# Kernel tuning notes

Hardware: AMD Instinct MI355X
Metric: run time of the kernel (lower is better)

The kernel has to match this reference:

```python
import jax, jax.numpy as jnp
import numpy as np

T, B, C, S = 1000, 64, 512, 100
BLANK = 0
SMOOTHING = 0.1
NEG = -1e30  # finite -inf sentinel (safe for logaddexp and grads)


def setup_inputs() -> dict:
    key = jax.random.key(0)
    k1, k2, k3 = jax.random.split(key, 3)
    logits = jax.random.normal(k1, (T, B, C), dtype=jnp.float32)
    # nn.CTCLoss expects log-probabilities over the class dim
    log_probs = jax.nn.log_softmax(logits, axis=-1)
    targets = jax.random.randint(k2, (B, S), 1, C, dtype=jnp.int32)  # avoid blank=0
    input_lengths = jnp.full((B,), T, dtype=jnp.int32)
    target_lengths = jax.random.randint(k3, (B,), S // 2, S + 1, dtype=jnp.int32)
    return {"log_probs": log_probs, "targets": targets,
            "input_lengths": input_lengths, "target_lengths": target_lengths}


def ctc_nll(log_probs, targets, input_lengths, target_lengths):
    """Per-sample CTC negative log-likelihood via log-domain alpha recursion."""
    Tt, Bb, Cc = log_probs.shape
    Ss = targets.shape[1]
    L = 2 * Ss + 1  # extended label sequence: blank t1 blank t2 ... blank
    ext = jnp.full((Bb, L), BLANK, dtype=targets.dtype).at[:, 1::2].set(targets)
    bidx = jnp.arange(Bb)[:, None]
    lp_ext = log_probs[:, bidx, ext]  # (T, B, L) emission log-probs along extended labels
    # skip transition s-2 -> s allowed iff label is non-blank and differs from label at s-2
    skip_ok = (jnp.arange(L)[None, :] >= 2) & (ext != BLANK) & (ext != jnp.roll(ext, 2, axis=1))

    alpha0 = jnp.full((Bb, L), NEG, dtype=log_probs.dtype)
    alpha0 = alpha0.at[:, 0].set(lp_ext[0, :, 0]).at[:, 1].set(lp_ext[0, :, 1])

    neg1 = jnp.full((Bb, 1), NEG, dtype=log_probs.dtype)
    neg2 = jnp.full((Bb, 2), NEG, dtype=log_probs.dtype)

    def step(alpha, xs):
        lp_t, t = xs
        s1 = jnp.concatenate([neg1, alpha[:, :-1]], axis=1)
        s2 = jnp.where(skip_ok, jnp.concatenate([neg2, alpha[:, :-2]], axis=1), NEG)
        new = jnp.logaddexp(jnp.logaddexp(alpha, s1), s2) + lp_t
        # freeze alpha once past this sample's input length
        alpha = jnp.where((t < input_lengths)[:, None], new, alpha)
        return alpha, None

    alphaT, _ = jax.lax.scan(step, alpha0, (lp_ext[1:], jnp.arange(1, Tt)))
    last = 2 * target_lengths  # index of final blank; last-1 is final label
    rows = jnp.arange(Bb)
    ll = jnp.logaddexp(alphaT[rows, last], alphaT[rows, last - 1])
    nll = -ll
    # zero_infinity=True: clamp non-finite (sentinel-scale) losses to 0
    return jnp.where(nll > 1e29, 0.0, nll)


def reference(log_probs, targets, input_lengths, target_lengths):
    nll = ctc_nll(log_probs, targets, input_lengths, target_lengths)
    # reduction='mean': divide each loss by its target length, then mean over batch
    base_loss = jnp.mean(nll / target_lengths.astype(log_probs.dtype))
    # entropy regularizer: -(p * log p).sum(-1).mean()
    entropy = -jnp.mean(jnp.sum(jnp.exp(log_probs) * log_probs, axis=-1))
    return (1.0 - SMOOTHING) * base_loss - SMOOTHING * entropy
```

## Files before the change

kernel.cpp:

```cpp
#include <hip/hip_runtime.h>

constexpr int   T_ = 1000, B_ = 64, C_ = 512, S_ = 100;
constexpr int   L_ = 2 * S_ + 1;
constexpr float NEGF = -1e30f;
constexpr int   PF = 21;
constexpr int   ENT_BLOCKS = 1984;
constexpr int   ROWB = B_ * C_ * 4;
constexpr int   ENT_W = ENT_BLOCKS * 4;
constexpr int   WS_N  = ENT_W + B_;
constexpr float K2    = 1.44269504088896340736f;
constexpr float LN2   = 0.69314718055994530942f;

#define GLOADI(dst, voff, sbase) \
  asm volatile("global_load_dword %0, %1, %2" : "+v"(dst) : "v"(voff), "s"(sbase))

__device__ __forceinline__ float fexp2(float x) {
#if __has_builtin(__builtin_amdgcn_exp2f)
  return __builtin_amdgcn_exp2f(x);
#else
  float r; asm("v_exp_f32 %0, %1" : "=v"(r) : "v"(x)); return r;
#endif
}

__device__ __forceinline__ float l2ae2(float a, float b) {
  float m = fmaxf(a, b);
  return m + __log2f(fexp2(a - m) + fexp2(b - m));
}
__device__ __forceinline__ float l2ae3(float a, float b, float c) {
  float m = fmaxf(fmaxf(a, b), c);
  return m + __log2f(fexp2(a - m) + fexp2(b - m) + fexp2(c - m));
}

#define RING(X) X(0) X(1) X(2) X(3) X(4) X(5) X(6) X(7) X(8) X(9) X(10) \
                X(11) X(12) X(13) X(14) X(15) X(16) X(17) X(18) X(19) X(20)

__global__ __launch_bounds__(256, 2) void ctc_fused_kernel(
    const float* __restrict__ lp,
    const int*   __restrict__ targets,
    const int*   __restrict__ in_len,
    const int*   __restrict__ tgt_len,
    float*       __restrict__ ws) {
  const int bid = blockIdx.x;

  if (bid < B_) {
    if (threadIdx.x >= 64) return;
    const int lane = threadIdx.x;
    const int b = bid;
    const int* tgt = targets + b * S_;

    const int s0 = lane * 4;
    const int i1 = lane * 2;
    const int e1 = (s0 + 1 < L_) ? tgt[i1] : 0;
    const int e3 = (s0 + 3 < L_) ? tgt[i1 + 1] : 0;
    const int ep = (lane > 0 && (i1 - 1) < S_) ? tgt[i1 - 1] : 0;
    const bool sk1 = (s0 + 1 >= 2) && (e1 != 0) && (e1 != ep);
    const bool sk3 = (e3 != 0) && (e3 != e1);

    const int len = in_len[b];
    const int tl  = tgt_len[b];

    const float* base = lp + (size_t)b * C_;

    float i0  = base[0];
    float i1v = base[e1];
    float a0 = (lane == 0) ? i0 * K2  : NEGF;
    float a1 = (lane == 0) ? i1v * K2 : NEGF;
    float a2 = NEGF, a3 = NEGF;
    asm volatile("" :: "v"(a0), "v"(a1));
    asm volatile("" :: "s"(len), "s"(tl));

    unsigned voffB = (unsigned)ROWB;
    unsigned voff1 = (unsigned)(ROWB + e1 * 4);
    unsigned voff3 = (unsigned)(ROWB + e3 * 4);

#define DECLR(J) float pb##J = 0.f, q1##J = 0.f, q3##J = 0.f;
    RING(DECLR)
#undef DECLR

    __builtin_amdgcn_s_setprio(1);

#define ISSUER(J) \
    GLOADI(pb##J, voffB, base); \
    GLOADI(q1##J, voff1, base); \
    GLOADI(q3##J, voff3, base); \
    voffB += ROWB; voff1 += ROWB; voff3 += ROWB;
    RING(ISSUER)
#undef ISSUER

#define STEPR(J) { \
    const int t = t0 + J; \
    asm volatile("s_waitcnt vmcnt(60)" ::: "memory"); \
    __builtin_amdgcn_sched_barrier(0); \
    const float lpb  = pb##J * K2; \
    const float lp1v = q1##J * K2; \
    const float lp3v = q3##J * K2; \
    float up1 = __shfl_up(a3, 1); \
    if (lane == 0) up1 = NEGF; \
    float n0 = l2ae2(a0, up1); \
    float n1 = l2ae3(a1, a0, sk1 ? up1 : NEGF); \
    float n2 = l2ae2(a2, a1); \
    float n3 = l2ae3(a3, a2, sk3 ? a1 : NEGF); \
    const bool upd = (t < len); \
    a0 = upd ? (n0 + lpb)  : a0; \
    a1 = upd ? (n1 + lp1v) : a1; \
    a2 = upd ? (n2 + lpb)  : a2; \
    a3 = upd ? (n3 + lp3v) : a3; \
    __builtin_amdgcn_sched_barrier(0); \
    GLOADI(pb##J, voffB, base); \
    GLOADI(q1##J, voff1, base); \
    GLOADI(q3##J, voff3, base); \
    const unsigned adv = (t + PF < T_ - 1) ? (unsigned)ROWB : 0u; \
    voffB += adv; voff1 += adv; voff3 += adv; \
  }
    for (int t0 = 1; t0 <= 1 + 47 * PF; t0 += PF) {
      RING(STEPR)
    }
#undef STEPR
    asm volatile("s_waitcnt vmcnt(0)" ::: "memory");
    __builtin_amdgcn_s_setprio(0);

    const int last = 2 * tl;
    const int lane_hi = last >> 2,       sub_hi = last & 3;
    const int lane_lo = (last - 1) >> 2, sub_lo = (last - 1) & 3;
    float cand_hi = (sub_hi == 0) ? a0 : (sub_hi == 1) ? a1 : (sub_hi == 2) ? a2 : a3;
    float cand_lo = (sub_lo == 0) ? a0 : (sub_lo == 1) ? a1 : (sub_lo == 2) ? a2 : a3;
    float vhi = __shfl(cand_hi, lane_hi);
    float vlo = __shfl(cand_lo, lane_lo);
    if (lane == 0) {
      float ll = LN2 * l2ae2(vhi, vlo);
      float nll = -ll;
      if (nll > 1e29f) nll = 0.0f;
      ws[ENT_W + b] = 0.9f * nll / ((float)tl * (float)B_);
    }
  } else {
    const int ebid = bid - B_;
    const size_t tid = (size_t)ebid * blockDim.x + threadIdx.x;
    const size_t nthreads = (size_t)ENT_BLOCKS * blockDim.x;
    const float4* v = (const float4*)lp;
    const size_t n4 = (size_t)T_ * B_ * C_ / 4;
    float s = 0.0f;
    for (size_t i = tid; i < n4; i += nthreads) {
      float4 x = v[i];
      s += __expf(x.x) * x.x + __expf(x.y) * x.y
         + __expf(x.z) * x.z + __expf(x.w) * x.w;
    }
    for (int o = 32; o > 0; o >>= 1) s += __shfl_down(s, o);
    if ((threadIdx.x & 63) == 0) {
      const int wslot = ebid * 4 + (int)(threadIdx.x >> 6);
      ws[wslot] = s;
    }
  }
}

__global__ __launch_bounds__(256) void finalize_kernel(
    const float* __restrict__ ws, float* __restrict__ out) {
  const float entScale = 0.1f / ((float)T_ * (float)B_);
  float acc = 0.0f;
  for (int i = threadIdx.x; i < WS_N; i += 256) {
    float v = ws[i];
    acc += (i < ENT_W) ? v * entScale : v;
  }
  for (int o = 32; o > 0; o >>= 1) acc += __shfl_down(acc, o);
  __shared__ float red[4];
  if ((threadIdx.x & 63) == 0) red[threadIdx.x >> 6] = acc;
  __syncthreads();
  if (threadIdx.x == 0) out[0] = red[0] + red[1] + red[2] + red[3];
}

extern "C" void kernel_launch(void* const* d_in, const int* in_sizes, int n_in,
                              void* d_out, int out_size, void* d_ws, size_t ws_size,
                              hipStream_t stream) {
  const float* lp  = (const float*)d_in[0];
  const int*   tg  = (const int*)d_in[1];
  const int*   il  = (const int*)d_in[2];
  const int*   tl  = (const int*)d_in[3];
  float*       ws  = (float*)d_ws;
  float*       out = (float*)d_out;

  dim3 grid(B_ + ENT_BLOCKS), block(256);
  ctc_fused_kernel<<<grid, block, 0, stream>>>(lp, tg, il, tl, ws);
  finalize_kernel<<<1, 256, 0, stream>>>(ws, out);
}
```

Measured before the change: 322.3 us.

## Stage CTC emission prefetch through an LDS ring via global_load_lds

```diff
diff --git a/kernel.cpp b/kernel.cpp
--- a/kernel.cpp
+++ b/kernel.cpp
@@ -3,16 +3,16 @@
 constexpr int   T_ = 1000, B_ = 64, C_ = 512, S_ = 100;
 constexpr int   L_ = 2 * S_ + 1;
 constexpr float NEGF = -1e30f;
-constexpr int   PF = 21;
+constexpr int   R_ = 16;
+constexpr int   SLOTB = 1024;
 constexpr int   ENT_BLOCKS = 1984;
-constexpr int   ROWB = B_ * C_ * 4;
 constexpr int   ENT_W = ENT_BLOCKS * 4;
 constexpr int   WS_N  = ENT_W + B_;
 constexpr float K2    = 1.44269504088896340736f;
 constexpr float LN2   = 0.69314718055994530942f;
 
-#define GLOADI(dst, voff, sbase) \
-  asm volatile("global_load_dword %0, %1, %2" : "+v"(dst) : "v"(voff), "s"(sbase))
+typedef __attribute__((address_space(1))) const void gvoid;
+typedef __attribute__((address_space(3))) void       lvoid;
 
 __device__ __forceinline__ float fexp2(float x) {
 #if __has_builtin(__builtin_amdgcn_exp2f)
@@ -24,23 +24,22 @@
 
 __device__ __forceinline__ float l2ae2(float a, float b) {
   float m = fmaxf(a, b);
-  return m + __log2f(fexp2(a - m) + fexp2(b - m));
+  float d = fminf(a, b) - m;
+  return m + __log2f(1.0f + fexp2(d));
 }
 __device__ __forceinline__ float l2ae3(float a, float b, float c) {
   float m = fmaxf(fmaxf(a, b), c);
   return m + __log2f(fexp2(a - m) + fexp2(b - m) + fexp2(c - m));
 }
 
-#define RING(X) X(0) X(1) X(2) X(3) X(4) X(5) X(6) X(7) X(8) X(9) X(10) \
-                X(11) X(12) X(13) X(14) X(15) X(16) X(17) X(18) X(19) X(20)
-
-__global__ __launch_bounds__(256, 2) void ctc_fused_kernel(
+__global__ __launch_bounds__(256) void ctc_fused_kernel(
     const float* __restrict__ lp,
     const int*   __restrict__ targets,
     const int*   __restrict__ in_len,
     const int*   __restrict__ tgt_len,
     float*       __restrict__ ws) {
   const int bid = blockIdx.x;
+  __shared__ char lds[R_ * SLOTB];
 
   if (bid < B_) {
     if (threadIdx.x >= 64) return;
@@ -69,54 +68,78 @@
     asm volatile("" :: "v"(a0), "v"(a1));
     asm volatile("" :: "s"(len), "s"(tl));
 
-    unsigned voffB = (unsigned)ROWB;
-    unsigned voff1 = (unsigned)(ROWB + e1 * 4);
-    unsigned voff3 = (unsigned)(ROWB + e3 * 4);
-
-#define DECLR(J) float pb##J = 0.f, q1##J = 0.f, q3##J = 0.f;
-    RING(DECLR)
-#undef DECLR
+    const int lane4 = lane * 4;
 
     __builtin_amdgcn_s_setprio(1);
 
-#define ISSUER(J) \
-    GLOADI(pb##J, voffB, base); \
-    GLOADI(q1##J, voff1, base); \
-    GLOADI(q3##J, voff3, base); \
-    voffB += ROWB; voff1 += ROWB; voff3 += ROWB;
-    RING(ISSUER)
-#undef ISSUER
-
-#define STEPR(J) { \
-    const int t = t0 + J; \
-    asm volatile("s_waitcnt vmcnt(60)" ::: "memory"); \
+#pragma unroll
+    for (int r = 1; r <= R_; ++r) {
+      const float* rowp = base + (size_t)r * (B_ * C_);
+      char* l0 = lds + (r & (R_ - 1)) * SLOTB;
+      __builtin_amdgcn_global_load_lds((gvoid*)rowp,        (lvoid*)l0,         4, 0, 0);
+      __builtin_amdgcn_global_load_lds((gvoid*)(rowp + e1), (lvoid*)(l0 + 256), 4, 0, 0);
+      __builtin_amdgcn_global_load_lds((gvoid*)(rowp + e3), (lvoid*)(l0 + 512), 4, 0, 0);
+    }
+    const float* rowp = base + (size_t)(R_ + 1) * (B_ * C_);
+
+    float pbA, p1A, p3A, pbB, p1B, p3B;
+    asm volatile("s_waitcnt vmcnt(45)" ::: "memory");
+    __builtin_amdgcn_sched_barrier(0);
+    asm volatile("ds_read_b32 %0, %3 offset:0\n\t"
+                 "ds_read_b32 %1, %3 offset:256\n\t"
+                 "ds_read_b32 %2, %3 offset:512"
+                 : "=&v"(pbA), "=&v"(p1A), "=&v"(p3A)
+                 : "v"(lane4 + 1 * SLOTB));
+    asm volatile("s_waitcnt vmcnt(42)" ::: "memory");
+    __builtin_amdgcn_sched_barrier(0);
+    asm volatile("ds_read_b32 %0, %3 offset:0\n\t"
+                 "ds_read_b32 %1, %3 offset:256\n\t"
+                 "ds_read_b32 %2, %3 offset:512"
+                 : "=&v"(pbB), "=&v"(p1B), "=&v"(p3B)
+                 : "v"(lane4 + 2 * SLOTB));
+
+    int t = 1;
+    int rowg   = R_ + 1;
+    int rd_off = 3 * SLOTB;
+    int wr_off = 1 * SLOTB;
+
+#define PHASE(PB, P1, P3) { \
+    asm volatile("s_waitcnt lgkmcnt(3)" ::: "memory"); \
     __builtin_amdgcn_sched_barrier(0); \
-    const float lpb  = pb##J * K2; \
-    const float lp1v = q1##J * K2; \
-    const float lp3v = q3##J * K2; \
-    float up1 = __shfl_up(a3, 1); \
-    if (lane == 0) up1 = NEGF; \
-    float n0 = l2ae2(a0, up1); \
-    float n1 = l2ae3(a1, a0, sk1 ? up1 : NEGF); \
-    float n2 = l2ae2(a2, a1); \
-    float n3 = l2ae3(a3, a2, sk3 ? a1 : NEGF); \
-    const bool upd = (t < len); \
-    a0 = upd ? (n0 + lpb)  : a0; \
-    a1 = upd ? (n1 + lp1v) : a1; \
-    a2 = upd ? (n2 + lpb)  : a2; \
-    a3 = upd ? (n3 + lp3v) : a3; \
+    if (t < len) {   \
+      const float lpb = PB * K2, lp1v = P1 * K2, lp3v = P3 * K2; \
+      float up1 = __shfl_up(a3, 1); \
+      if (lane == 0) up1 = NEGF; \
+      float n0 = l2ae2(a0, up1); \
+      float n1 = l2ae3(a1, a0, sk1 ? up1 : NEGF); \
+      float n2 = l2ae2(a2, a1); \
+      float n3 = l2ae3(a3, a2, sk3 ? a1 : NEGF); \
+      a0 = n0 + lpb; a1 = n1 + lp1v; a2 = n2 + lpb; a3 = n3 + lp3v; \
+    } \
+    { char* l0 = lds + wr_off; \
+      __builtin_amdgcn_global_load_lds((gvoid*)rowp,        (lvoid*)l0,         4, 0, 0); \
+      __builtin_amdgcn_global_load_lds((gvoid*)(rowp + e1), (lvoid*)(l0 + 256), 4, 0, 0); \
+      __builtin_amdgcn_global_load_lds((gvoid*)(rowp + e3), (lvoid*)(l0 + 512), 4, 0, 0); \
+      if (rowg < T_ - 1) { rowp += B_ * C_; ++rowg; } \
+      wr_off = (wr_off + SLOTB) & (R_ * SLOTB - 1); } \
+    asm volatile("s_waitcnt vmcnt(42)" ::: "memory");   \
     __builtin_amdgcn_sched_barrier(0); \
-    GLOADI(pb##J, voffB, base); \
-    GLOADI(q1##J, voff1, base); \
-    GLOADI(q3##J, voff3, base); \
-    const unsigned adv = (t + PF < T_ - 1) ? (unsigned)ROWB : 0u; \
-    voffB += adv; voff1 += adv; voff3 += adv; \
-  }
-    for (int t0 = 1; t0 <= 1 + 47 * PF; t0 += PF) {
-      RING(STEPR)
-    }
-#undef STEPR
-    asm volatile("s_waitcnt vmcnt(0)" ::: "memory");
+    asm volatile("ds_read_b32 %0, %3 offset:0\n\t" \
+                 "ds_read_b32 %1, %3 offset:256\n\t" \
+                 "ds_read_b32 %2, %3 offset:512" \
+                 : "=&v"(PB), "=&v"(P1), "=&v"(P3) \
+                 : "v"(lane4 + rd_off)); \
+    rd_off = (rd_off + SLOTB) & (R_ * SLOTB - 1); \
+    ++t; }
+
+#pragma clang loop unroll(disable)
+    for (int it = 0; it < 504; ++it) {
+      PHASE(pbA, p1A, p3A)
+      PHASE(pbB, p1B, p3B)
+    }
+#undef PHASE
+
+    asm volatile("s_waitcnt vmcnt(0) lgkmcnt(0)" ::: "memory");
     __builtin_amdgcn_s_setprio(0);
 
     const int last = 2 * tl;
```

After: 386.9 us. +20.0%, slower.
